# Kernel optimization log

Hardware: AMD Instinct MI355X
Metric: run time of the kernel (lower is better)

## Reference

```python
import jax, jax.numpy as jnp
import numpy as np

HID = 128
N_BLOCKS = 50000
ATOMS_PER_BLOCK = 8
N_ATOMS = N_BLOCKS * ATOMS_PER_BLOCK  # 400k
N_EDGES = 800000
ATOM_VOCAB = 100
N_BOND_TYPES = 5
CORRUPT_RATIO = 0.1


def setup_inputs() -> dict:
    key = jax.random.key(0)
    ks = jax.random.split(key, 20)
    A = jax.random.randint(ks[0], (N_ATOMS,), 0, ATOM_VOCAB)
    src = jax.random.randint(ks[1], (N_EDGES,), 0, N_ATOMS)
    dst = jax.random.randint(ks[2], (N_EDGES,), 0, N_ATOMS)
    btyp = jax.random.randint(ks[3], (N_EDGES,), 0, N_BOND_TYPES)
    bonds = jnp.stack([src, dst, btyp], axis=1)  # [E, 3]
    block_ids = jnp.arange(N_ATOMS) // ATOMS_PER_BLOCK  # atom -> block, sorted
    generate_mask = jax.random.uniform(ks[4], (N_BLOCKS,)) < 0.5
    position_ids = jax.random.randint(ks[5], (N_BLOCKS,), 0, 1024)
    is_aa = jax.random.randint(ks[6], (N_BLOCKS,), 0, 2)
    corrupt_rand = jax.random.uniform(ks[7], (N_BLOCKS,))
    s = 0.02
    p = {
        'atom_embed': jax.random.normal(ks[8], (ATOM_VOCAB, HID)) * s,
        'bond_embed': jax.random.normal(ks[9], (N_BOND_TYPES, HID)) * s,
        'is_aa_embed': jax.random.normal(ks[10], (2, HID)) * s,
        'gine_w1': jax.random.normal(ks[11], (HID, HID)) * s,
        'gine_b1': jnp.zeros((HID,)),
        'gine_w2': jax.random.normal(ks[12], (HID, HID)) * s,
        'gine_b2': jnp.zeros((HID,)),
        'mlp_w0': jax.random.normal(ks[13], (3 * HID, HID)) * s,
        'mlp_b0': jnp.zeros((HID,)),
        'mlp_w1': jax.random.normal(ks[14], (HID, HID)) * s,
        'mlp_b1': jnp.zeros((HID,)),
        'mlp_w2': jax.random.normal(ks[15], (HID, HID)) * s,
        'mlp_b2': jnp.zeros((HID,)),
    }
    return dict(A=A, bonds=bonds, block_ids=block_ids, generate_mask=generate_mask,
                position_ids=position_ids, is_aa=is_aa, corrupt_rand=corrupt_rand, **p)


def _sinusoidal(pos, dim):
    # standard sinusoidal position embedding, [N] -> [N, dim]
    inv_freq = 1.0 / (10000.0 ** (jnp.arange(0, dim, 2, dtype=jnp.float32) / dim))
    ang = pos.astype(jnp.float32)[:, None] * inv_freq[None, :]
    return jnp.concatenate([jnp.sin(ang), jnp.cos(ang)], axis=-1)


def reference(A, bonds, block_ids, generate_mask, position_ids, is_aa, corrupt_rand,
              atom_embed, bond_embed, is_aa_embed,
              gine_w1, gine_b1, gine_w2, gine_b2,
              mlp_w0, mlp_b0, mlp_w1, mlp_b1, mlp_w2, mlp_b2):
    src, dst, btyp = bonds[:, 0], bonds[:, 1], bonds[:, 2]
    # context atoms: atoms whose block is NOT being generated
    ctx = ~generate_mask[block_ids]                       # [N_atoms]
    valid = (ctx[src] & ctx[dst]).astype(jnp.float32)     # edge-select mask (== dropping bonds)
    # GINEConv: msg = relu(x_j + e), aggregated by sum at dst, eps = 0
    Hn = atom_embed[A]                                    # [N_atoms, H]
    edge_attr = bond_embed[btyp]                          # [E, H]
    msg = jax.nn.relu(Hn[src] + edge_attr) * valid[:, None]
    agg = jax.ops.segment_sum(msg, dst, num_segments=N_ATOMS)
    h = Hn + agg
    h = jax.nn.relu(h @ gine_w1 + gine_b1) @ gine_w2 + gine_b2
    # std-conserving scatter mean: sum / sqrt(count)
    blk_sum = jax.ops.segment_sum(h, block_ids, num_segments=N_BLOCKS)
    cnt = jax.ops.segment_sum(jnp.ones((N_ATOMS,), jnp.float32), block_ids, num_segments=N_BLOCKS)
    topo = blk_sum / jnp.sqrt(jnp.maximum(cnt, 1.0))[:, None]
    topo = jnp.where(generate_mask[:, None], 0.0, topo)
    # is_aa embedding with corruption on generated blocks
    corrupt = generate_mask & (corrupt_rand < CORRUPT_RATIO)
    is_aa_e = is_aa_embed[jnp.where(corrupt, 0, is_aa)]
    pos_e = _sinusoidal(position_ids, HID)
    x = jnp.concatenate([pos_e, topo, is_aa_e], axis=-1)  # [N_blocks, 3H]
    # 3-layer cond MLP (dropout inactive in eval)
    x = jax.nn.relu(x @ mlp_w0 + mlp_b0)
    x = jax.nn.relu(x @ mlp_w1 + mlp_b1)
    cond = x @ mlp_w2 + mlp_b2
    return cond
```

## Files before the change

kernel.cpp:

```cpp
#include <hip/hip_runtime.h>
#include <hip/hip_bf16.h>

#define NBLK  50000
#define NATOM 400000
#define NEDGE 800000
#define CAP   40

typedef __bf16 bf16x8 __attribute__((ext_vector_type(8)));
typedef float  f32x4  __attribute__((ext_vector_type(4)));

#define MCNT_OFF 0UL
#define EW1_OFF  200000UL
#define REC_OFF  251200UL
#define T_OFF    4251200UL
#define PW_OFF   4507200UL
#define W2T_OFF  4769344UL
#define M1T_OFF  4802112UL
#define M2T_OFF  4834880UL
#define AAW_OFF  4867648UL
#define GM_OFF   4869696UL
#define FLAG_OFF 4919696UL
#define TOPO_OFF 4919712UL
#define WS_NEED  18403840UL

#define RS8 0.35355339059327373f

#define MFMA(a,b,c) __builtin_amdgcn_mfma_f32_16x16x32_bf16((a),(b),(c),0,0,0)

__device__ inline f32x4 splat4(float v){ f32x4 r; r[0]=v; r[1]=v; r[2]=v; r[3]=v; return r; }
__device__ inline float scrub(float v){ return (v==v && v<1e30f && v>-1e30f) ? v : 0.f; }

__global__ void k_sniff(const void* gm_raw, char* ws) {
  __shared__ int big;
  if (threadIdx.x == 0) big = 0;
  __syncthreads();
  const unsigned* gw = (const unsigned*)gm_raw;
  for (int i = threadIdx.x; i < 12500; i += 256)
    if (gw[i] > 1u) big = 1;
  __syncthreads();
  if (threadIdx.x == 0) *(int*)(ws + FLAG_OFF) = big;
}

__global__ void k_prep(const float* atom_embed, const float* bond_embed,
                       const float* m0, const float* m1, const float* m2,
                       const float* g2, const float* gb2, const float* aa_embed,
                       const void* gm_raw, const int* __restrict__ bonds,
                       const int* __restrict__ A, char* ws) {
  int b = blockIdx.x, t = threadIdx.x;
  if (b < 100) {
    float ae = atom_embed[b*128 + t];
    float* T = (float*)(ws + T_OFF);
    for (int bo = 0; bo < 5; ++bo) {
      float v = ae + bond_embed[bo*128 + t];
      T[(b*5 + bo)*128 + t] = v > 0.f ? v : 0.f;
    }
  } else if (b < 116) {
    int wb = b - 100;
    const float* src; __bf16* dst; int r0;
    if (wb < 8) { src = m1; dst = (__bf16*)(ws + M1T_OFF); r0 = wb*16; }
    else        { src = m2; dst = (__bf16*)(ws + M2T_OFF); r0 = (wb-8)*16; }
    for (int rr = 0; rr < 16; ++rr) {
      int r = r0 + rr;
      dst[t*128 + r] = (__bf16)src[r*128 + t];
    }
  } else if (b < 166) {
    int anyBig = *(const int*)(ws + FLAG_OFF);
    int base = (b - 116) * 1000;
    unsigned char* gu = (unsigned char*)(ws + GM_OFF);
    if (anyBig) {
      const unsigned char* gb = (const unsigned char*)gm_raw;
      for (int i = t; i < 1000; i += 128) gu[base+i] = gb[base+i] ? 1 : 0;
    } else {
      const int* gi = (const int*)gm_raw;
      for (int i = t; i < 1000; i += 128) gu[base+i] = gi[base+i] ? 1 : 0;
    }
  } else if (b < 1190) {
    int p = b - 166;
    __shared__ float s[128];
    int c = t & 63;
    float invf = exp2f((float)c * -0.20762050593046012f);
    float ang = (float)p * invf;
    s[t] = (t < 64) ? __sinf(ang) : __cosf(ang);
    __syncthreads();
    float acc = 0.f;
    #pragma unroll 4
    for (int j = 0; j < 128; ++j) acc += s[j] * m0[j*128 + t];
    ((__bf16*)(ws + PW_OFF))[p*128 + t] = (__bf16)acc;
  } else if (b < 1318) {
    int r = b - 1190;
    float acc = 0.f;
    #pragma unroll 4
    for (int j = 0; j < 128; ++j) acc += g2[r*128 + j] * m0[(128+j)*128 + t];
    ((__bf16*)(ws + W2T_OFF))[t*128 + r] = (__bf16)(acc * RS8);
  } else if (b < 1322) {
    int sf = b - 1318, sel = sf & 1, f = sf >> 1;
    float acc = 0.f;
    #pragma unroll 4
    for (int j = 0; j < 128; ++j) acc += aa_embed[sel*128 + j] * m0[(256+j)*128 + t];
    if (f) {
      float cacc = 0.f;
      #pragma unroll 4
      for (int j = 0; j < 128; ++j) cacc += gb2[j] * m0[(128+j)*128 + t];
      acc += 8.0f * RS8 * cacc;
    }
    ((float*)(ws + AAW_OFF))[sf*128 + t] = acc;
  } else {
    int anyBig = *(const int*)(ws + FLAG_OFF);
    const unsigned char* g8 = (const unsigned char*)gm_raw;
    const int* g32 = (const int*)gm_raw;
    long base = ((long)(b - 1322)*128 + t)*8;
    #pragma unroll 2
    for (int h = 0; h < 2; ++h) {
      long e4 = base + h*4;
      if (e4 >= NEDGE) break;
      const int4* bp = (const int4*)(bonds + e4*3);
      int4 w0 = bp[0], w1 = bp[1], w2 = bp[2];
      int srcs[4] = {w0.x, w0.w, w1.z, w2.y};
      int dsts[4] = {w0.y, w1.x, w1.w, w2.z};
      int bts[4]  = {w0.z, w1.y, w2.x, w2.w};
      #pragma unroll
      for (int i = 0; i < 4; ++i) {
        int sm_ = srcs[i] >> 3, dm = dsts[i] >> 3;
        int bad = anyBig ? ((int)g8[sm_] | (int)g8[dm]) : (g32[sm_] | g32[dm]);
        if (bad) continue;
        int slot = atomicAdd((int*)(ws + MCNT_OFF) + dm, 1);
        if (slot >= 0 && slot < CAP)
          ((unsigned short*)(ws + REC_OFF))[dm*CAP + slot] =
            (unsigned short)((A[srcs[i]]*5 + bts[i])*8 + (dsts[i] & 7));
      }
    }
  }
}

__global__ void k_prep2(const float* atom_embed, const float* g1, const float* gb1,
                        char* ws) {
  int b = blockIdx.x, t = threadIdx.x;
  float s0 = 0.f, s1 = 0.f, s2 = 0.f, s3 = 0.f;
  const float* row = (b < 100) ? (atom_embed + b*128) : ((float*)(ws + T_OFF) + (b-100)*128);
  #pragma unroll 4
  for (int k = 0; k < 128; k += 4) {
    s0 += row[k+0] * g1[(k+0)*128 + t];
    s1 += row[k+1] * g1[(k+1)*128 + t];
    s2 += row[k+2] * g1[(k+2)*128 + t];
    s3 += row[k+3] * g1[(k+3)*128 + t];
  }
  float s = (s0 + s1) + (s2 + s3);
  if (b < 100) {
    ((float*)(ws + EW1_OFF))[b*128 + t] = s + gb1[t];
  } else {
    __syncthreads();
    ((float*)(ws + T_OFF))[(b-100)*128 + t] = s;
  }
}

__launch_bounds__(256, 6)
__global__ void k_gather5(char* ws, const int* __restrict__ A) {
  const int tid = threadIdx.x;
  const int lane = tid & 63, wid = tid >> 6;
  const int mol = blockIdx.x*4 + wid;
  const int a_l = lane >> 3, q8 = lane & 7;
  const unsigned char* gm = (const unsigned char*)(ws + GM_OFF);

  f32x4 a0 = splat4(0.f), a1 = splat4(0.f), a2 = splat4(0.f), a3 = splat4(0.f);
  f32x4 b0 = splat4(0.f), b1 = splat4(0.f), b2 = splat4(0.f), b3 = splat4(0.f);
  if (!gm[mol]) {
    const int* cnt = (const int*)(ws + MCNT_OFF);
    const unsigned* rec32 = (const unsigned*)(ws + REC_OFF);
    const unsigned short* rec16 = (const unsigned short*)(ws + REC_OFF);
    const float* EW1 = (const float*)(ws + EW1_OFF);
    const float* TW1 = (const float*)(ws + T_OFF);
    int n = cnt[mol];
    if (n > CAP) n = CAP;
    if (n < 0) n = 0;
    int aT = A[mol*8 + a_l];
    const f32x4* ep = (const f32x4*)(EW1 + aT*128 + q8*16);
    a0 = ep[0]; a1 = ep[1]; a2 = ep[2]; a3 = ep[3];
    const int base32 = mol*(CAP/2);
    int i = 0;
    for (; i + 4 <= n; i += 4) {
      unsigned pr0 = rec32[base32 + (i >> 1)];
      unsigned pr1 = rec32[base32 + (i >> 1) + 1];
      int rv0 = pr0 & 0xFFFF, rv1 = pr0 >> 16;
      int rv2 = pr1 & 0xFFFF, rv3 = pr1 >> 16;
      int p0 = rv0 >> 3, p1 = rv1 >> 3, p2 = rv2 >> 3, p3 = rv3 >> 3;
      if (p0 < 500 && (rv0 & 7) == a_l) {
        const f32x4* tp = (const f32x4*)(TW1 + p0*128 + q8*16);
        a0 += tp[0]; a1 += tp[1]; a2 += tp[2]; a3 += tp[3];
      }
      if (p1 < 500 && (rv1 & 7) == a_l) {
        const f32x4* tp = (const f32x4*)(TW1 + p1*128 + q8*16);
        b0 += tp[0]; b1 += tp[1]; b2 += tp[2]; b3 += tp[3];
      }
      if (p2 < 500 && (rv2 & 7) == a_l) {
        const f32x4* tp = (const f32x4*)(TW1 + p2*128 + q8*16);
        a0 += tp[0]; a1 += tp[1]; a2 += tp[2]; a3 += tp[3];
      }
      if (p3 < 500 && (rv3 & 7) == a_l) {
        const f32x4* tp = (const f32x4*)(TW1 + p3*128 + q8*16);
        b0 += tp[0]; b1 += tp[1]; b2 += tp[2]; b3 += tp[3];
      }
    }
    for (; i < n; ++i) {
      int rv = rec16[mol*CAP + i];
      int p = rv >> 3;
      if (p < 500 && (rv & 7) == a_l) {
        const f32x4* tp = (const f32x4*)(TW1 + p*128 + q8*16);
        b0 += tp[0]; b1 += tp[1]; b2 += tp[2]; b3 += tp[3];
      }
    }
  }
  #pragma unroll
  for (int k = 0; k < 4; ++k) {
    float x0 = fmaxf(a0[k] + b0[k], 0.f), x1 = fmaxf(a1[k] + b1[k], 0.f);
    float x2 = fmaxf(a2[k] + b2[k], 0.f), x3 = fmaxf(a3[k] + b3[k], 0.f);
    x0 += __shfl_xor(x0, 8);  x1 += __shfl_xor(x1, 8);
    x2 += __shfl_xor(x2, 8);  x3 += __shfl_xor(x3, 8);
    x0 += __shfl_xor(x0, 16); x1 += __shfl_xor(x1, 16);
    x2 += __shfl_xor(x2, 16); x3 += __shfl_xor(x3, 16);
    x0 += __shfl_xor(x0, 32); x1 += __shfl_xor(x1, 32);
    x2 += __shfl_xor(x2, 32); x3 += __shfl_xor(x3, 32);
    a0[k] = x0; a1[k] = x1; a2[k] = x2; a3[k] = x3;
  }
  if (a_l == 0) {
    bf16x8 o0, o1;
    #pragma unroll
    for (int k = 0; k < 4; ++k) {
      o0[k] = (__bf16)a0[k]; o0[k+4] = (__bf16)a1[k];
      o1[k] = (__bf16)a2[k]; o1[k+4] = (__bf16)a3[k];
    }
    char* dst = ws + TOPO_OFF + (long)mol*256 + q8*32;
    *(bf16x8*)dst = o0;
    *(bf16x8*)(dst + 16) = o1;
  }
}

__device__ inline void gemm4(const char* sm, int aoff, const __bf16* wt,
                             const float* bias, int lane, int wave, f32x4 acc[4][2]) {
  const int colA = wave*32 + (lane & 15);
  const int k0   = (lane >> 4) * 8;
  float bb0 = bias[colA], bb1 = bias[colA + 16];
  #pragma unroll
  for (int m = 0; m < 4; ++m) { acc[m][0] = splat4(bb0); acc[m][1] = splat4(bb1); }
  #pragma unroll
  for (int kb = 0; kb < 4; ++kb) {
    bf16x8 b0 = *(const bf16x8*)(wt + colA*128 + kb*32 + k0);
    bf16x8 b1 = *(const bf16x8*)(wt + (colA+16)*128 + kb*32 + k0);
    #pragma unroll
    for (int m = 0; m < 4; ++m) {
      int rA = m*16 + (lane & 15);
      int byte = aoff + rA*256 + (((kb*64) + k0*2) ^ ((rA & 7) << 4));
      bf16x8 a = *(const bf16x8*)(sm + byte);
      acc[m][0] = MFMA(a, b0, acc[m][0]);
      acc[m][1] = MFMA(a, b1, acc[m][1]);
    }
  }
}

__device__ inline void stor4(char* sm, int off, f32x4 acc[4][2],
                             int lane, int wave, bool do_relu) {
  #pragma unroll
  for (int m = 0; m < 4; ++m)
  #pragma unroll
  for (int nf = 0; nf < 2; ++nf)
  #pragma unroll
  for (int r = 0; r < 4; ++r) {
    float v = acc[m][nf][r];
    if (do_relu && v < 0.f) v = 0.f;
    int row = m*16 + (lane >> 4)*4 + r;
    int col = wave*32 + nf*16 + (lane & 15);
    int byte = off + row*256 + ((col*2) ^ ((row & 7) << 4));
    *(__bf16*)(sm + byte) = (__bf16)v;
  }
}

__launch_bounds__(256)
__global__ void k_mlp3(char* ws, const int* __restrict__ pos_ids,
                       const int* __restrict__ is_aa, const float* cr,
                       const float* mb0, const float* mb1, const float* mb2,
                       float* __restrict__ out) {
  __shared__ __align__(16) char sm[32768];
  const int tid = threadIdx.x, lane = tid & 63, wave = tid >> 6;
  const int r0 = blockIdx.x * 64;
  const unsigned char* gm = (const unsigned char*)(ws + GM_OFF);
  const __bf16* topo_pre = (const __bf16*)(ws + TOPO_OFF);

  for (int i = 0; i < 4; ++i) {
    int idx = tid + i*256;
    int row = idx >> 4, c = idx & 15;
    int mol = r0 + row;
    bf16x8 v;
    #pragma unroll
    for (int j = 0; j < 8; ++j) v[j] = (__bf16)0.f;
    if (mol < NBLK) v = *(const bf16x8*)(topo_pre + (long)mol*128 + c*8);
    int byte = row*256 + ((c*16) ^ ((row & 7) << 4));
    *(bf16x8*)(sm + byte) = v;
  }
  if (tid < 64) {
    int mol = r0 + tid, packed = 0;
    if (mol < NBLK) {
      int g = gm[mol];
      int corrupt = g && (cr[mol] < 0.1f);
      int sel = corrupt ? 0 : is_aa[mol];
      packed = pos_ids[mol] | (sel << 12) | ((g ? 0 : 1) << 13);
    }
    *(int*)(sm + 16384 + tid*4) = packed;
  }
  __syncthreads();

  f32x4 acc[4][2];
  gemm4(sm, 0, (const __bf16*)(ws + W2T_OFF), mb0, lane, wave, acc);
  {
    const __bf16* PW = (const __bf16*)(ws + PW_OFF);
    const float* AAW = (const float*)(ws + AAW_OFF);
    #pragma unroll
    for (int m = 0; m < 4; ++m)
    #pragma unroll
    for (int r = 0; r < 4; ++r) {
      int row = m*16 + (lane >> 4)*4 + r;
      int packed = *(const int*)(sm + 16384 + row*4);
      int pid = packed & 0xFFF, sf = (packed >> 12) & 3;
      #pragma unroll
      for (int nf = 0; nf < 2; ++nf) {
        int col = wave*32 + nf*16 + (lane & 15);
        float v = acc[m][nf][r] + (float)PW[pid*128 + col] + AAW[sf*128 + col];
        acc[m][nf][r] = fmaxf(v, 0.f);
      }
    }
  }
  __syncthreads();
  stor4(sm, 0, acc, lane, wave, false);
  __syncthreads();

  gemm4(sm, 0, (const __bf16*)(ws + M1T_OFF), mb1, lane, wave, acc);
  stor4(sm, 16384, acc, lane, wave, true);
  __syncthreads();

  gemm4(sm, 16384, (const __bf16*)(ws + M2T_OFF), mb2, lane, wave, acc);
  #pragma unroll
  for (int m = 0; m < 4; ++m)
  #pragma unroll
  for (int nf = 0; nf < 2; ++nf)
  #pragma unroll
  for (int r = 0; r < 4; ++r) {
    int row = m*16 + (lane >> 4)*4 + r;
    int col = wave*32 + nf*16 + (lane & 15);
    int mol = r0 + row;
    if (mol < NBLK) out[(long)mol*128 + col] = scrub(acc[m][nf][r]);
  }
}

extern "C" void kernel_launch(void* const* d_in, const int* in_sizes, int n_in,
                              void* d_out, int out_size, void* d_ws, size_t ws_size,
                              hipStream_t stream) {
  if (ws_size < WS_NEED) return;
  const int* A      = (const int*)d_in[0];
  const int* bonds  = (const int*)d_in[1];
  const void* gm    = d_in[3];
  const int* pos    = (const int*)d_in[4];
  const int* isaa   = (const int*)d_in[5];
  const float* cr   = (const float*)d_in[6];
  const float* atom_embed = (const float*)d_in[7];
  const float* bond_embed = (const float*)d_in[8];
  const float* aa_embed   = (const float*)d_in[9];
  const float* g1  = (const float*)d_in[10];
  const float* gb1 = (const float*)d_in[11];
  const float* g2  = (const float*)d_in[12];
  const float* gb2 = (const float*)d_in[13];
  const float* m0  = (const float*)d_in[14];
  const float* mb0 = (const float*)d_in[15];
  const float* m1  = (const float*)d_in[16];
  const float* mb1 = (const float*)d_in[17];
  const float* m2  = (const float*)d_in[18];
  const float* mb2 = (const float*)d_in[19];
  char* ws = (char*)d_ws;

  hipMemsetAsync(ws + MCNT_OFF, 0, (size_t)NBLK*4, stream);
  k_sniff  <<<1, 256, 0, stream>>>(gm, ws);
  k_prep   <<<2104, 128, 0, stream>>>(atom_embed, bond_embed, m0, m1, m2,
                                      g2, gb2, aa_embed, gm, bonds, A, ws);
  k_prep2  <<<600, 128, 0, stream>>>(atom_embed, g1, gb1, ws);
  k_gather5<<<NBLK/4, 256, 0, stream>>>(ws, A);
  k_mlp3   <<<(NBLK + 63)/64, 256, 0, stream>>>(ws, pos, isaa, cr,
                                                mb0, mb1, mb2, (float*)d_out);
}
```

Before: 113.8 us.

## Merge prep kernels, skip generated blocks in gather, halve MLP tile rows

Folds the second prep kernel into the first so the atom and bond-pair projections through the first GINE weight are computed directly, each block staging its input row in shared memory. The gather kernel now returns early for generated blocks and relies on a new memset that zeroes the topo buffer, rather than computing and writing zeros. The MLP kernel processes 32 rows per workgroup instead of 64, using half the shared memory and twice as many workgroups. Together these remove a launch and a dependency stage and cut gather writes, at the cost of an extra memset of the topo buffer and less weight reuse per MLP workgroup.

New measurement: 121.8 us. 1.07x slower.

```diff
diff --git a/kernel.cpp b/kernel.cpp
--- a/kernel.cpp
+++ b/kernel.cpp
@@ -12,7 +12,7 @@
 #define MCNT_OFF 0UL
 #define EW1_OFF  200000UL
 #define REC_OFF  251200UL
-#define T_OFF    4251200UL
+#define TW1_OFF  4251200UL
 #define PW_OFF   4507200UL
 #define W2T_OFF  4769344UL
 #define M1T_OFF  4802112UL
@@ -42,30 +42,24 @@
 }
 
 __global__ void k_prep(const float* atom_embed, const float* bond_embed,
+                       const float* g1, const float* gb1,
                        const float* m0, const float* m1, const float* m2,
                        const float* g2, const float* gb2, const float* aa_embed,
                        const void* gm_raw, const int* __restrict__ bonds,
                        const int* __restrict__ A, char* ws) {
   int b = blockIdx.x, t = threadIdx.x;
-  if (b < 100) {
-    float ae = atom_embed[b*128 + t];
-    float* T = (float*)(ws + T_OFF);
-    for (int bo = 0; bo < 5; ++bo) {
-      float v = ae + bond_embed[bo*128 + t];
-      T[(b*5 + bo)*128 + t] = v > 0.f ? v : 0.f;
-    }
-  } else if (b < 116) {
-    int wb = b - 100;
+  __shared__ float rr[128];
+  if (b < 16) {
     const float* src; __bf16* dst; int r0;
-    if (wb < 8) { src = m1; dst = (__bf16*)(ws + M1T_OFF); r0 = wb*16; }
-    else        { src = m2; dst = (__bf16*)(ws + M2T_OFF); r0 = (wb-8)*16; }
-    for (int rr = 0; rr < 16; ++rr) {
-      int r = r0 + rr;
+    if (b < 8) { src = m1; dst = (__bf16*)(ws + M1T_OFF); r0 = b*16; }
+    else       { src = m2; dst = (__bf16*)(ws + M2T_OFF); r0 = (b-8)*16; }
+    for (int rro = 0; rro < 16; ++rro) {
+      int r = r0 + rro;
       dst[t*128 + r] = (__bf16)src[r*128 + t];
     }
-  } else if (b < 166) {
+  } else if (b < 66) {
     int anyBig = *(const int*)(ws + FLAG_OFF);
-    int base = (b - 116) * 1000;
+    int base = (b - 16) * 1000;
     unsigned char* gu = (unsigned char*)(ws + GM_OFF);
     if (anyBig) {
       const unsigned char* gb = (const unsigned char*)gm_raw;
@@ -74,41 +68,11 @@
       const int* gi = (const int*)gm_raw;
       for (int i = t; i < 1000; i += 128) gu[base+i] = gi[base+i] ? 1 : 0;
     }
-  } else if (b < 1190) {
-    int p = b - 166;
-    __shared__ float s[128];
-    int c = t & 63;
-    float invf = exp2f((float)c * -0.20762050593046012f);
-    float ang = (float)p * invf;
-    s[t] = (t < 64) ? __sinf(ang) : __cosf(ang);
-    __syncthreads();
-    float acc = 0.f;
-    #pragma unroll 4
-    for (int j = 0; j < 128; ++j) acc += s[j] * m0[j*128 + t];
-    ((__bf16*)(ws + PW_OFF))[p*128 + t] = (__bf16)acc;
-  } else if (b < 1318) {
-    int r = b - 1190;
-    float acc = 0.f;
-    #pragma unroll 4
-    for (int j = 0; j < 128; ++j) acc += g2[r*128 + j] * m0[(128+j)*128 + t];
-    ((__bf16*)(ws + W2T_OFF))[t*128 + r] = (__bf16)(acc * RS8);
-  } else if (b < 1322) {
-    int sf = b - 1318, sel = sf & 1, f = sf >> 1;
-    float acc = 0.f;
-    #pragma unroll 4
-    for (int j = 0; j < 128; ++j) acc += aa_embed[sel*128 + j] * m0[(256+j)*128 + t];
-    if (f) {
-      float cacc = 0.f;
-      #pragma unroll 4
-      for (int j = 0; j < 128; ++j) cacc += gb2[j] * m0[(128+j)*128 + t];
-      acc += 8.0f * RS8 * cacc;
-    }
-    ((float*)(ws + AAW_OFF))[sf*128 + t] = acc;
-  } else {
+  } else if (b < 848) {
     int anyBig = *(const int*)(ws + FLAG_OFF);
     const unsigned char* g8 = (const unsigned char*)gm_raw;
     const int* g32 = (const int*)gm_raw;
-    long base = ((long)(b - 1322)*128 + t)*8;
+    long base = ((long)(b - 66)*128 + t)*8;
     #pragma unroll 2
     for (int h = 0; h < 2; ++h) {
       long e4 = base + h*4;
@@ -129,27 +93,58 @@
             (unsigned short)((A[srcs[i]]*5 + bts[i])*8 + (dsts[i] & 7));
       }
     }
-  }
-}
-
-__global__ void k_prep2(const float* atom_embed, const float* g1, const float* gb1,
-                        char* ws) {
-  int b = blockIdx.x, t = threadIdx.x;
-  float s0 = 0.f, s1 = 0.f, s2 = 0.f, s3 = 0.f;
-  const float* row = (b < 100) ? (atom_embed + b*128) : ((float*)(ws + T_OFF) + (b-100)*128);
-  #pragma unroll 4
-  for (int k = 0; k < 128; k += 4) {
-    s0 += row[k+0] * g1[(k+0)*128 + t];
-    s1 += row[k+1] * g1[(k+1)*128 + t];
-    s2 += row[k+2] * g1[(k+2)*128 + t];
-    s3 += row[k+3] * g1[(k+3)*128 + t];
-  }
-  float s = (s0 + s1) + (s2 + s3);
-  if (b < 100) {
-    ((float*)(ws + EW1_OFF))[b*128 + t] = s + gb1[t];
+  } else if (b < 948) {
+    int a = b - 848;
+    rr[t] = atom_embed[a*128 + t];
+    __syncthreads();
+    float acc = 0.f;
+    #pragma unroll 4
+    for (int k = 0; k < 128; ++k) acc += rr[k] * g1[k*128 + t];
+    ((float*)(ws + EW1_OFF))[a*128 + t] = acc + gb1[t];
+  } else if (b < 1448) {
+    int r = b - 948, a = r / 5, bo = r % 5;
+    rr[t] = fmaxf(atom_embed[a*128 + t] + bond_embed[bo*128 + t], 0.f);
+    __syncthreads();
+    float acc = 0.f;
+    #pragma unroll 4
+    for (int k = 0; k < 128; ++k) acc += rr[k] * g1[k*128 + t];
+    ((float*)(ws + TW1_OFF))[r*128 + t] = acc;
+  } else if (b < 2472) {
+    int p = b - 1448;
+    int c = t & 63;
+    float invf = exp2f((float)c * -0.20762050593046012f);
+    float ang = (float)p * invf;
+    rr[t] = (t < 64) ? __sinf(ang) : __cosf(ang);
+    __syncthreads();
+    float acc = 0.f;
+    #pragma unroll 4
+    for (int j = 0; j < 128; ++j) acc += rr[j] * m0[j*128 + t];
+    ((__bf16*)(ws + PW_OFF))[p*128 + t] = (__bf16)acc;
+  } else if (b < 2600) {
+    int r = b - 2472;
+    rr[t] = g2[r*128 + t];
+    __syncthreads();
+    float acc = 0.f;
+    #pragma unroll 4
+    for (int j = 0; j < 128; ++j) acc += rr[j] * m0[(128+j)*128 + t];
+    ((__bf16*)(ws + W2T_OFF))[t*128 + r] = (__bf16)(acc * RS8);
   } else {
-    __syncthreads();
-    ((float*)(ws + T_OFF))[(b-100)*128 + t] = s;
+    int sf = b - 2600, sel = sf & 1, f = sf >> 1;
+    rr[t] = aa_embed[sel*128 + t];
+    __syncthreads();
+    float acc = 0.f;
+    #pragma unroll 4
+    for (int j = 0; j < 128; ++j) acc += rr[j] * m0[(256+j)*128 + t];
+    if (f) {
+      __syncthreads();
+      rr[t] = gb2[t];
+      __syncthreads();
+      float cacc = 0.f;
+      #pragma unroll 4
+      for (int j = 0; j < 128; ++j) cacc += rr[j] * m0[(128+j)*128 + t];
+      acc += 8.0f * RS8 * cacc;
+    }
+    ((float*)(ws + AAW_OFF))[sf*128 + t] = acc;
   }
 }
 
@@ -160,53 +155,51 @@
   const int mol = blockIdx.x*4 + wid;
   const int a_l = lane >> 3, q8 = lane & 7;
   const unsigned char* gm = (const unsigned char*)(ws + GM_OFF);
-
-  f32x4 a0 = splat4(0.f), a1 = splat4(0.f), a2 = splat4(0.f), a3 = splat4(0.f);
+  if (gm[mol]) return;
+
+  const int* cnt = (const int*)(ws + MCNT_OFF);
+  const unsigned* rec32 = (const unsigned*)(ws + REC_OFF);
+  const unsigned short* rec16 = (const unsigned short*)(ws + REC_OFF);
+  const float* EW1 = (const float*)(ws + EW1_OFF);
+  const float* TW1 = (const float*)(ws + TW1_OFF);
+  int n = cnt[mol];
+  if (n > CAP) n = CAP;
+  if (n < 0) n = 0;
+  int aT = A[mol*8 + a_l];
+  const f32x4* ep = (const f32x4*)(EW1 + aT*128 + q8*16);
+  f32x4 a0 = ep[0], a1 = ep[1], a2 = ep[2], a3 = ep[3];
   f32x4 b0 = splat4(0.f), b1 = splat4(0.f), b2 = splat4(0.f), b3 = splat4(0.f);
-  if (!gm[mol]) {
-    const int* cnt = (const int*)(ws + MCNT_OFF);
-    const unsigned* rec32 = (const unsigned*)(ws + REC_OFF);
-    const unsigned short* rec16 = (const unsigned short*)(ws + REC_OFF);
-    const float* EW1 = (const float*)(ws + EW1_OFF);
-    const float* TW1 = (const float*)(ws + T_OFF);
-    int n = cnt[mol];
-    if (n > CAP) n = CAP;
-    if (n < 0) n = 0;
-    int aT = A[mol*8 + a_l];
-    const f32x4* ep = (const f32x4*)(EW1 + aT*128 + q8*16);
-    a0 = ep[0]; a1 = ep[1]; a2 = ep[2]; a3 = ep[3];
-    const int base32 = mol*(CAP/2);
-    int i = 0;
-    for (; i + 4 <= n; i += 4) {
-      unsigned pr0 = rec32[base32 + (i >> 1)];
-      unsigned pr1 = rec32[base32 + (i >> 1) + 1];
-      int rv0 = pr0 & 0xFFFF, rv1 = pr0 >> 16;
-      int rv2 = pr1 & 0xFFFF, rv3 = pr1 >> 16;
-      int p0 = rv0 >> 3, p1 = rv1 >> 3, p2 = rv2 >> 3, p3 = rv3 >> 3;
-      if (p0 < 500 && (rv0 & 7) == a_l) {
-        const f32x4* tp = (const f32x4*)(TW1 + p0*128 + q8*16);
-        a0 += tp[0]; a1 += tp[1]; a2 += tp[2]; a3 += tp[3];
-      }
-      if (p1 < 500 && (rv1 & 7) == a_l) {
-        const f32x4* tp = (const f32x4*)(TW1 + p1*128 + q8*16);
-        b0 += tp[0]; b1 += tp[1]; b2 += tp[2]; b3 += tp[3];
-      }
-      if (p2 < 500 && (rv2 & 7) == a_l) {
-        const f32x4* tp = (const f32x4*)(TW1 + p2*128 + q8*16);
-        a0 += tp[0]; a1 += tp[1]; a2 += tp[2]; a3 += tp[3];
-      }
-      if (p3 < 500 && (rv3 & 7) == a_l) {
-        const f32x4* tp = (const f32x4*)(TW1 + p3*128 + q8*16);
-        b0 += tp[0]; b1 += tp[1]; b2 += tp[2]; b3 += tp[3];
-      }
-    }
-    for (; i < n; ++i) {
-      int rv = rec16[mol*CAP + i];
-      int p = rv >> 3;
-      if (p < 500 && (rv & 7) == a_l) {
-        const f32x4* tp = (const f32x4*)(TW1 + p*128 + q8*16);
-        b0 += tp[0]; b1 += tp[1]; b2 += tp[2]; b3 += tp[3];
-      }
+  const int base32 = mol*(CAP/2);
+  int i = 0;
+  for (; i + 4 <= n; i += 4) {
+    unsigned pr0 = rec32[base32 + (i >> 1)];
+    unsigned pr1 = rec32[base32 + (i >> 1) + 1];
+    int rv0 = pr0 & 0xFFFF, rv1 = pr0 >> 16;
+    int rv2 = pr1 & 0xFFFF, rv3 = pr1 >> 16;
+    int p0 = rv0 >> 3, p1 = rv1 >> 3, p2 = rv2 >> 3, p3 = rv3 >> 3;
+    if (p0 < 500 && (rv0 & 7) == a_l) {
+      const f32x4* tp = (const f32x4*)(TW1 + p0*128 + q8*16);
+      a0 += tp[0]; a1 += tp[1]; a2 += tp[2]; a3 += tp[3];
+    }
+    if (p1 < 500 && (rv1 & 7) == a_l) {
+      const f32x4* tp = (const f32x4*)(TW1 + p1*128 + q8*16);
+      b0 += tp[0]; b1 += tp[1]; b2 += tp[2]; b3 += tp[3];
+    }
+    if (p2 < 500 && (rv2 & 7) == a_l) {
+      const f32x4* tp = (const f32x4*)(TW1 + p2*128 + q8*16);
+      a0 += tp[0]; a1 += tp[1]; a2 += tp[2]; a3 += tp[3];
+    }
+    if (p3 < 500 && (rv3 & 7) == a_l) {
+      const f32x4* tp = (const f32x4*)(TW1 + p3*128 + q8*16);
+      b0 += tp[0]; b1 += tp[1]; b2 += tp[2]; b3 += tp[3];
+    }
+  }
+  for (; i < n; ++i) {
+    int rv = rec16[mol*CAP + i];
+    int p = rv >> 3;
+    if (p < 500 && (rv & 7) == a_l) {
+      const f32x4* tp = (const f32x4*)(TW1 + p*128 + q8*16);
+      b0 += tp[0]; b1 += tp[1]; b2 += tp[2]; b3 += tp[3];
     }
   }
   #pragma unroll
@@ -234,19 +227,19 @@
   }
 }
 
-__device__ inline void gemm4(const char* sm, int aoff, const __bf16* wt,
-                             const float* bias, int lane, int wave, f32x4 acc[4][2]) {
+__device__ inline void gemm2(const char* sm, int aoff, const __bf16* wt,
+                             const float* bias, int lane, int wave, f32x4 acc[2][2]) {
   const int colA = wave*32 + (lane & 15);
   const int k0   = (lane >> 4) * 8;
   float bb0 = bias[colA], bb1 = bias[colA + 16];
   #pragma unroll
-  for (int m = 0; m < 4; ++m) { acc[m][0] = splat4(bb0); acc[m][1] = splat4(bb1); }
+  for (int m = 0; m < 2; ++m) { acc[m][0] = splat4(bb0); acc[m][1] = splat4(bb1); }
   #pragma unroll
   for (int kb = 0; kb < 4; ++kb) {
     bf16x8 b0 = *(const bf16x8*)(wt + colA*128 + kb*32 + k0);
     bf16x8 b1 = *(const bf16x8*)(wt + (colA+16)*128 + kb*32 + k0);
     #pragma unroll
-    for (int m = 0; m < 4; ++m) {
+    for (int m = 0; m < 2; ++m) {
       int rA = m*16 + (lane & 15);
       int byte = aoff + rA*256 + (((kb*64) + k0*2) ^ ((rA & 7) << 4));
       bf16x8 a = *(const bf16x8*)(sm + byte);
@@ -256,10 +249,10 @@
   }
 }
 
-__device__ inline void stor4(char* sm, int off, f32x4 acc[4][2],
+__device__ inline void stor2(char* sm, int off, f32x4 acc[2][2],
                              int lane, int wave, bool do_relu) {
   #pragma unroll
-  for (int m = 0; m < 4; ++m)
+  for (int m = 0; m < 2; ++m)
   #pragma unroll
   for (int nf = 0; nf < 2; ++nf)
   #pragma unroll
@@ -278,13 +271,13 @@
                        const int* __restrict__ is_aa, const float* cr,
                        const float* mb0, const float* mb1, const float* mb2,
                        float* __restrict__ out) {
-  __shared__ __align__(16) char sm[32768];
+  __shared__ __align__(16) char sm[16512];
   const int tid = threadIdx.x, lane = tid & 63, wave = tid >> 6;
-  const int r0 = blockIdx.x * 64;
+  const int r0 = blockIdx.x * 32;
   const unsigned char* gm = (const unsigned char*)(ws + GM_OFF);
   const __bf16* topo_pre = (const __bf16*)(ws + TOPO_OFF);
 
-  for (int i = 0; i < 4; ++i) {
+  for (int i = 0; i < 2; ++i) {
     int idx = tid + i*256;
     int row = idx >> 4, c = idx & 15;
     int mol = r0 + row;
@@ -295,7 +288,7 @@
     int byte = row*256 + ((c*16) ^ ((row & 7) << 4));
     *(bf16x8*)(sm + byte) = v;
   }
-  if (tid < 64) {
+  if (tid < 32) {
     int mol = r0 + tid, packed = 0;
     if (mol < NBLK) {
       int g = gm[mol];
@@ -307,13 +300,13 @@
   }
   __syncthreads();
 
-  f32x4 acc[4][2];
-  gemm4(sm, 0, (const __bf16*)(ws + W2T_OFF), mb0, lane, wave, acc);
+  f32x4 acc[2][2];
+  gemm2(sm, 0, (const __bf16*)(ws + W2T_OFF), mb0, lane, wave, acc);
   {
     const __bf16* PW = (const __bf16*)(ws + PW_OFF);
     const float* AAW = (const float*)(ws + AAW_OFF);
     #pragma unroll
-    for (int m = 0; m < 4; ++m)
+    for (int m = 0; m < 2; ++m)
     #pragma unroll
     for (int r = 0; r < 4; ++r) {
       int row = m*16 + (lane >> 4)*4 + r;
@@ -328,16 +321,16 @@
     }
   }
   __syncthreads();
-  stor4(sm, 0, acc, lane, wave, false);
-  __syncthreads();
-
-  gemm4(sm, 0, (const __bf16*)(ws + M1T_OFF), mb1, lane, wave, acc);
-  stor4(sm, 16384, acc, lane, wave, true);
-  __syncthreads();
-
-  gemm4(sm, 16384, (const __bf16*)(ws + M2T_OFF), mb2, lane, wave, acc);
-  #pragma unroll
-  for (int m = 0; m < 4; ++m)
+  stor2(sm, 0, acc, lane, wave, false);
+  __syncthreads();
+
+  gemm2(sm, 0, (const __bf16*)(ws + M1T_OFF), mb1, lane, wave, acc);
+  stor2(sm, 8192, acc, lane, wave, true);
+  __syncthreads();
+
+  gemm2(sm, 8192, (const __bf16*)(ws + M2T_OFF), mb2, lane, wave, acc);
+  #pragma unroll
+  for (int m = 0; m < 2; ++m)
   #pragma unroll
   for (int nf = 0; nf < 2; ++nf)
   #pragma unroll
@@ -375,11 +368,11 @@
   char* ws = (char*)d_ws;
 
   hipMemsetAsync(ws + MCNT_OFF, 0, (size_t)NBLK*4, stream);
+  hipMemsetAsync(ws + TOPO_OFF, 0, (size_t)NBLK*256, stream);
   k_sniff  <<<1, 256, 0, stream>>>(gm, ws);
-  k_prep   <<<2104, 128, 0, stream>>>(atom_embed, bond_embed, m0, m1, m2,
+  k_prep   <<<2604, 128, 0, stream>>>(atom_embed, bond_embed, g1, gb1, m0, m1, m2,
                                       g2, gb2, aa_embed, gm, bonds, A, ws);
-  k_prep2  <<<600, 128, 0, stream>>>(atom_embed, g1, gb1, ws);
   k_gather5<<<NBLK/4, 256, 0, stream>>>(ws, A);
-  k_mlp3   <<<(NBLK + 63)/64, 256, 0, stream>>>(ws, pos, isaa, cr,
+  k_mlp3   <<<(NBLK + 31)/32, 256, 0, stream>>>(ws, pos, isaa, cr,
                                                 mb0, mb1, mb2, (float*)d_out);
 }
```
